# Optimization experiments

Measured on AMD Instinct MI355X. Metric: run time of the kernel, lower is better.

Reference implementation:

```python
import jax, jax.numpy as jnp
import numpy as np

DIM = 32
DN = ('NCDHW', 'OIDHW', 'NCDHW')


def _dwconv(x, w, b, pad, dil):
    # depthwise 3D conv, x: [N, C, D, H, W], w: [C, 1, kd, kh, kw]
    y = jax.lax.conv_general_dilated(
        x, w, window_strides=(1, 1, 1),
        padding=[(pad[0], pad[0]), (pad[1], pad[1]), (pad[2], pad[2])],
        rhs_dilation=dil, dimension_numbers=DN,
        feature_group_count=x.shape[1])
    return y + b[None, :, None, None, None]


def setup_inputs() -> dict:
    key = jax.random.key(0)
    ks = jax.random.split(key, 11)
    B, T, C, D, H, W = 1, 8, DIM, 32, 64, 64
    x = jax.random.normal(ks[0], (B, T, C, D, H, W), dtype=jnp.float32)
    s = 0.1
    w0z = jax.random.normal(ks[1], (C, 1, 3, 1, 1), dtype=jnp.float32) * s
    b0z = jax.random.normal(ks[2], (C,), dtype=jnp.float32) * s
    w0x = jax.random.normal(ks[3], (C, 1, 1, 3, 1), dtype=jnp.float32) * s
    b0x = jax.random.normal(ks[4], (C,), dtype=jnp.float32) * s
    w0y = jax.random.normal(ks[5], (C, 1, 1, 1, 3), dtype=jnp.float32) * s
    b0y = jax.random.normal(ks[6], (C,), dtype=jnp.float32) * s
    wsz = jax.random.normal(ks[7], (C, 1, 5, 1, 1), dtype=jnp.float32) * s
    bsz = jax.random.normal(ks[8], (C,), dtype=jnp.float32) * s
    wp = jax.random.normal(ks[9], (C, C, 1, 1, 1), dtype=jnp.float32) * s
    bp = jax.random.normal(ks[10], (C,), dtype=jnp.float32) * s
    return {"x": x, "w0z": w0z, "b0z": b0z, "w0x": w0x, "b0x": b0x,
            "w0y": w0y, "b0y": b0y, "wsz": wsz, "bsz": bsz,
            "wp": wp, "bp": bp}


def reference(x, w0z, b0z, w0x, b0x, w0y, b0y, wsz, bsz, wp, bp):
    B, T, C, D, H, W = x.shape
    h = x.reshape(B * T, C, D, H, W)  # TimeDistributed flatten
    res = h
    h = _dwconv(h, w0z, b0z, (1, 0, 0), (1, 1, 1))
    h = _dwconv(h, w0x, b0x, (0, 1, 0), (1, 1, 1))
    h = _dwconv(h, w0y, b0y, (0, 0, 1), (1, 1, 1))
    # forward applies conv_spatial_z three times (faithful to source)
    for _ in range(3):
        h = _dwconv(h, wsz, bsz, (4, 0, 0), (2, 1, 1))
    # pointwise 1x1x1 conv (full channel mixing)
    h = jax.lax.conv_general_dilated(
        h, wp, window_strides=(1, 1, 1),
        padding=[(0, 0)] * 3, dimension_numbers=DN)
    h = h + bp[None, :, None, None, None]
    out = res * h
    return out.reshape(B, T, C, D, H, W)
```

## Files before the change

### kernel.cpp

```cpp
#include <hip/hip_runtime.h>

constexpr int NT = 8;
constexpr int C  = 32;
constexpr int D  = 32;
constexpr int H  = 64;
constexpr int W  = 64;
constexpr int ROWS = 4;
constexpr int SP = D * H * W;
constexpr int HW = H * W;

typedef unsigned int u32;

static __device__ __forceinline__ u32 f2bf(float f) {
    u32 u = __float_as_uint(f);
    return (u + 0x7fffu + ((u >> 16) & 1u)) >> 16;
}
static __device__ __forceinline__ float bf_lo(u32 v) { return __uint_as_float(v << 16); }
static __device__ __forceinline__ float bf_hi(u32 v) { return __uint_as_float(v & 0xffff0000u); }

__global__ __launch_bounds__(256, 4)
void dw_chain(const float* __restrict__ x,
              const float* __restrict__ w0z, const float* __restrict__ b0z,
              const float* __restrict__ w0x, const float* __restrict__ b0x,
              const float* __restrict__ w0y, const float* __restrict__ b0y,
              const float* __restrict__ wsz, const float* __restrict__ bsz,
              u32* __restrict__ hws)
{
    const int rr  = blockIdx.x;
    const int lid = (rr & 7) * (NT * C * (H / ROWS) / 8) + (rr >> 3);
    const int htile = lid % (H / ROWS);
    const int c     = (lid / (H / ROWS)) % C;
    const int n     = lid / ((H / ROWS) * C);

    const int tid = threadIdx.x;
    const int w   = tid & 63;
    const int hg  = __builtin_amdgcn_readfirstlane(htile * ROWS + (tid >> 6));

    const float* xc = x + ((size_t)n * C + c) * SP;

    const float wz0 = w0z[c*3+0], wz1 = w0z[c*3+1], wz2 = w0z[c*3+2];
    const float wx1 = w0x[c*3+1];
    const float wy0 = w0y[c*3+0], wy1 = w0y[c*3+1], wy2 = w0y[c*3+2];
    const float bz = b0z[c], bx = b0x[c], by = b0y[c], bs = bsz[c];
    float wsk[5];
    #pragma unroll
    for (int k = 0; k < 5; ++k) wsk[k] = wsz[c*5+k];

    const float wxk0 = (hg > 0)     ? w0x[c*3+0] : 0.f;
    const float wxk2 = (hg < H - 1) ? w0x[c*3+2] : 0.f;
    const int   hm = (hg > 0)     ? hg - 1 : 0;
    const int   hp = (hg < H - 1) ? hg + 1 : H - 1;

    const float* p0 = xc + (size_t)hm * W;
    const float* p1 = xc + (size_t)hg * W;
    const float* p2 = xc + (size_t)hp * W;

    float hrow[D];
    #pragma unroll
    for (int d = 0; d < D; ++d) {
        const float a0 = p0[(size_t)d * HW + w];
        const float a1 = p1[(size_t)d * HW + w];
        const float a2 = p2[(size_t)d * HW + w];
        hrow[d] = wxk0 * a0 + wx1 * a1 + wxk2 * a2;
    }

    const float cb = bx + (wxk0 + wx1 + wxk2) * bz;
    float acc2[D];
    #pragma unroll
    for (int d = 0; d < D; ++d) {
        float t = cb + wz1 * hrow[d];
        if (d > 0)     t += wz0 * hrow[d - 1];
        if (d < D - 1) t += wz2 * hrow[d + 1];
        acc2[d] = t;
    }

    const bool has_l = (w > 0), has_r = (w < W - 1);
    float acc3[D];
    #pragma unroll
    for (int d = 0; d < D; ++d) {
        float left  = __shfl_up(acc2[d], 1);
        float right = __shfl_down(acc2[d], 1);
        float t = by + wy1 * acc2[d];
        if (has_l) t += wy0 * left;
        if (has_r) t += wy2 * right;
        acc3[d] = t;
    }

    #pragma unroll
    for (int it = 0; it < 3; ++it) {
        float s[D];
        #pragma unroll
        for (int d = 0; d < D; ++d) {
            float t = bs;
            #pragma unroll
            for (int k = 0; k < 5; ++k) {
                int j = d + 2 * k - 4;
                if (j >= 0 && j < D) t += wsk[k] * acc3[j];
            }
            s[d] = t;
        }
        #pragma unroll
        for (int d = 0; d < D; ++d) acc3[d] = s[d];
    }

    u32* hc = hws + ((size_t)(n * C + c) * (D / 2)) * HW + (size_t)hg * W;
    #pragma unroll
    for (int k = 0; k < D / 2; ++k)
        hc[(size_t)k * HW + w] = f2bf(acc3[2*k]) | (f2bf(acc3[2*k+1]) << 16);
}

__global__ __launch_bounds__(256)
void pw_mul(const float* __restrict__ x,
            const u32* __restrict__ hws,
            const float* __restrict__ wp, const float* __restrict__ bp,
            float* __restrict__ out)
{
    const int b    = blockIdx.x;
    const int n    = b & 7;
    const int pid  = (b >> 3) * 256 + threadIdx.x;
    const int dp   = pid >> 12;
    const int sphw = pid & 4095;

    const u32* hp = hws + ((size_t)(n * C) * (D / 2) + dp) * HW + sphw;

    float v0[C], v1[C];
    #pragma unroll
    for (int ci = 0; ci < C; ++ci) {
        const u32 u = hp[(size_t)ci * (D / 2) * HW];
        v0[ci] = bf_lo(u);
        v1[ci] = bf_hi(u);
    }

    const size_t i0base = (size_t)n * C * SP + (size_t)(2 * dp) * HW + sphw;

    for (int co = 0; co < C; ++co) {
        float y0 = bp[co], y1 = bp[co];
        #pragma unroll
        for (int ci = 0; ci < C; ++ci) {
            const float wv = wp[co * C + ci];
            y0 += wv * v0[ci];
            y1 += wv * v1[ci];
        }
        const size_t ia = i0base + (size_t)co * SP;
        const size_t ib = ia + (size_t)HW;
        out[ia] = x[ia] * y0;
        out[ib] = x[ib] * y1;
    }
}

extern "C" void kernel_launch(void* const* d_in, const int* in_sizes, int n_in,
                              void* d_out, int out_size, void* d_ws, size_t ws_size,
                              hipStream_t stream)
{
    const float* x   = (const float*)d_in[0];
    const float* w0z = (const float*)d_in[1];
    const float* b0z = (const float*)d_in[2];
    const float* w0x = (const float*)d_in[3];
    const float* b0x = (const float*)d_in[4];
    const float* w0y = (const float*)d_in[5];
    const float* b0y = (const float*)d_in[6];
    const float* wsz = (const float*)d_in[7];
    const float* bsz = (const float*)d_in[8];
    const float* wp  = (const float*)d_in[9];
    const float* bp  = (const float*)d_in[10];
    float* out = (float*)d_out;
    u32* hws = (u32*)d_ws;

    const int gridA = NT * C * (H / ROWS);
    dw_chain<<<gridA, 256, 0, stream>>>(x, w0z, b0z, w0x, b0x, w0y, b0y,
                                        wsz, bsz, hws);

    const int gridB = NT * (D / 2) * HW / 256;
    pw_mul<<<gridB, 256, 0, stream>>>(x, hws, wp, bp, out);
}
```

Before: 109.4 us.

## Stage bf16 intermediate in output buffer and compute pointwise stage in place

The depthwise chain now writes its packed bf16 intermediate straight into the output buffer instead of a separate workspace. The pointwise kernel is re-tiled so each 512-thread block owns 32 HW columns across all depth pairs for one sample. It reads every intermediate value for those columns, synchronises, then overwrites the same columns with the final result. This removes the separate workspace footprint and aims for better cache reuse of the lines that get overwritten. In exchange, contiguous access shrinks to 32-element segments, and correctness depends on the block-local column ownership and the barrier.

```diff
diff --git a/kernel.cpp b/kernel.cpp
--- a/kernel.cpp
+++ b/kernel.cpp
@@ -8,6 +8,7 @@
 constexpr int ROWS = 4;
 constexpr int SP = D * H * W;
 constexpr int HW = H * W;
+constexpr int NREG = C * D * HW;
 
 typedef unsigned int u32;
 
@@ -24,7 +25,7 @@
               const float* __restrict__ w0x, const float* __restrict__ b0x,
               const float* __restrict__ w0y, const float* __restrict__ b0y,
               const float* __restrict__ wsz, const float* __restrict__ bsz,
-              u32* __restrict__ hws)
+              u32* __restrict__ hout)
 {
     const int rr  = blockIdx.x;
     const int lid = (rr & 7) * (NT * C * (H / ROWS) / 8) + (rr >> 3);
@@ -103,35 +104,41 @@
         for (int d = 0; d < D; ++d) acc3[d] = s[d];
     }
 
-    u32* hc = hws + ((size_t)(n * C + c) * (D / 2)) * HW + (size_t)hg * W;
+    u32* hc = hout + (size_t)n * NREG + (size_t)(c * (D / 2)) * HW
+                   + (size_t)hg * W;
     #pragma unroll
     for (int k = 0; k < D / 2; ++k)
         hc[(size_t)k * HW + w] = f2bf(acc3[2*k]) | (f2bf(acc3[2*k+1]) << 16);
 }
 
-__global__ __launch_bounds__(256)
+__global__ __launch_bounds__(512, 4)
 void pw_mul(const float* __restrict__ x,
-            const u32* __restrict__ hws,
             const float* __restrict__ wp, const float* __restrict__ bp,
-            float* __restrict__ out)
+            u32* __restrict__ io)
 {
     const int b    = blockIdx.x;
-    const int n    = b & 7;
-    const int pid  = (b >> 3) * 256 + threadIdx.x;
-    const int dp   = pid >> 12;
-    const int sphw = pid & 4095;
+    const int n    = b >> 7;
+    const int R0   = (b & 127) * 32;
+    const int tid  = threadIdx.x;
+    const int dp   = tid >> 5;
+    const int j    = tid & 31;
+    const int sphw = R0 + j;
 
-    const u32* hp = hws + ((size_t)(n * C) * (D / 2) + dp) * HW + sphw;
+    const u32* hn = io + (size_t)n * NREG;
 
     float v0[C], v1[C];
     #pragma unroll
     for (int ci = 0; ci < C; ++ci) {
-        const u32 u = hp[(size_t)ci * (D / 2) * HW];
+        const u32 u = hn[(size_t)(ci * (D / 2) + dp) * HW + sphw];
         v0[ci] = bf_lo(u);
         v1[ci] = bf_hi(u);
     }
 
-    const size_t i0base = (size_t)n * C * SP + (size_t)(2 * dp) * HW + sphw;
+    __syncthreads();
+
+    float* on = (float*)io + (size_t)n * NREG;
+    const float* xn = x + (size_t)n * NREG;
+    const size_t base0 = (size_t)(2 * dp) * HW + sphw;
 
     for (int co = 0; co < C; ++co) {
         float y0 = bp[co], y1 = bp[co];
@@ -141,10 +148,10 @@
             y0 += wv * v0[ci];
             y1 += wv * v1[ci];
         }
-        const size_t ia = i0base + (size_t)co * SP;
+        const size_t ia = (size_t)co * SP + base0;
         const size_t ib = ia + (size_t)HW;
-        out[ia] = x[ia] * y0;
-        out[ib] = x[ib] * y1;
+        on[ia] = xn[ia] * y0;
+        on[ib] = xn[ib] * y1;
     }
 }
 
@@ -163,13 +170,12 @@
     const float* bsz = (const float*)d_in[8];
     const float* wp  = (const float*)d_in[9];
     const float* bp  = (const float*)d_in[10];
-    float* out = (float*)d_out;
-    u32* hws = (u32*)d_ws;
+    u32* out = (u32*)d_out;
 
     const int gridA = NT * C * (H / ROWS);
     dw_chain<<<gridA, 256, 0, stream>>>(x, w0z, b0z, w0x, b0x, w0y, b0y,
-                                        wsz, bsz, hws);
+                                        wsz, bsz, out);
 
-    const int gridB = NT * (D / 2) * HW / 256;
-    pw_mul<<<gridB, 256, 0, stream>>>(x, hws, wp, bp, out);
+    const int gridB = NT * (HW / 32);
+    pw_mul<<<gridB, 512, 0, stream>>>(x, wp, bp, out);
 }
```

Result: slower. 166.2 us (+51.9%).
